# Kernel tuning notes

Measured on AMD Instinct MI355X. Metric: run time of the kernel, lower is better.

The kernel has to match this reference:

```python
import jax, jax.numpy as jnp
import numpy as np

EMBED_DIM = 256
N_COMPONENTS = 50
SIGMA = 1.0
B, N = 4, 4096


def setup_inputs() -> dict:
    key = jax.random.key(0)
    ks = jax.random.split(key, 7)
    d1, d2 = EMBED_DIM // 2, EMBED_DIM // 4  # 128, 64
    s = lambda fan_in: 1.0 / np.sqrt(fan_in)
    return {
        "embeddings": jax.random.normal(ks[0], (B, N, EMBED_DIM), dtype=jnp.float32),
        "W1": jax.random.uniform(ks[1], (EMBED_DIM, d1), jnp.float32, -s(EMBED_DIM), s(EMBED_DIM)),
        "b1": jax.random.uniform(ks[2], (d1,), jnp.float32, -s(EMBED_DIM), s(EMBED_DIM)),
        "W2": jax.random.uniform(ks[3], (d1, d2), jnp.float32, -s(d1), s(d1)),
        "b2": jax.random.uniform(ks[4], (d2,), jnp.float32, -s(d1), s(d1)),
        "W3": jax.random.uniform(ks[5], (d2, N_COMPONENTS), jnp.float32, -s(d2), s(d2)),
        "b3": jax.random.uniform(ks[6], (N_COMPONENTS,), jnp.float32, -s(d2), s(d2)),
    }


def reference(embeddings, W1, b1, W2, b2, W3, b3):
    # MLP projection: embed_dim -> embed_dim//2 -> embed_dim//4 -> n_components
    h = jax.nn.relu(jnp.einsum("bnd,df->bnf", embeddings, W1) + b1)
    h = jax.nn.relu(jnp.einsum("bnd,df->bnf", h, W2) + b2)
    z = jnp.einsum("bnd,df->bnf", h, W3) + b3  # (B, N, n_components)

    # Gaussian kernel from pairwise squared L2 distances: ||a-b||^2 = |a|^2 + |b|^2 - 2 a.b
    sq = jnp.sum(z * z, axis=-1)  # (B, N)
    dist = sq[:, :, None] + sq[:, None, :] - 2.0 * jnp.einsum("bik,bjk->bij", z, z)
    dist = jnp.maximum(dist, 0.0)
    kernel = jnp.exp(-dist / (2.0 * SIGMA ** 2))  # (B, N, N)

    # directed matrix: softmax over last dim, add epsilon, renormalize
    directed = jax.nn.softmax(kernel / SIGMA, axis=-1)
    directed = directed + 1e-6
    directed = directed / jnp.sum(directed, axis=-1, keepdims=True)
    return directed
```

## Files before the change

### kernel.cpp

```cpp
#include <hip/hip_runtime.h>
#include <cstdint>

#define ED 256
#define D1 128
#define D2 64
#define NC 50
#define NB 4
#define NN 4096
#define R1 16
#define TIB 8
#define JT 8
#define PTH 512

__global__ __launch_bounds__(256) void mlp_kernel(
    const float* __restrict__ emb,
    const float* __restrict__ W1, const float* __restrict__ b1,
    const float* __restrict__ W2, const float* __restrict__ b2,
    const float* __restrict__ W3, const float* __restrict__ b3,
    float* __restrict__ zT, float* __restrict__ sq)
{
    __shared__ __align__(16) float se[R1*ED];
    __shared__ __align__(16) float sh1[R1*D1];
    __shared__ __align__(16) float sh2[R1*D2];
    __shared__ __align__(16) float sz[R1*NC];
    const int t = threadIdx.x;
    const long row0 = (long)blockIdx.x * R1;

    {
        const float4* g4 = (const float4*)(emb + row0*ED);
        float4* s4 = (float4*)se;
        #pragma unroll
        for (int k = 0; k < (R1*ED/4)/256; k++)
            s4[t + k*256] = g4[t + k*256];
    }
    __syncthreads();

    {
        const int f = t & (D1-1);
        const int half = t >> 7;
        float acc[8];
        const float bias = b1[f];
        #pragma unroll
        for (int rr = 0; rr < 8; rr++) acc[rr] = bias;
        for (int d = 0; d < ED; d += 4) {
            const float w0 = W1[(d+0)*D1 + f];
            const float w1 = W1[(d+1)*D1 + f];
            const float w2 = W1[(d+2)*D1 + f];
            const float w3 = W1[(d+3)*D1 + f];
            #pragma unroll
            for (int rr = 0; rr < 8; rr++) {
                const float4 e = *(const float4*)&se[(half*8+rr)*ED + d];
                acc[rr] = fmaf(e.x, w0, acc[rr]);
                acc[rr] = fmaf(e.y, w1, acc[rr]);
                acc[rr] = fmaf(e.z, w2, acc[rr]);
                acc[rr] = fmaf(e.w, w3, acc[rr]);
            }
        }
        #pragma unroll
        for (int rr = 0; rr < 8; rr++)
            sh1[(half*8+rr)*D1 + f] = fmaxf(acc[rr], 0.0f);
    }
    __syncthreads();

    {
        const int f = t & (D2-1);
        const int g = t >> 6;
        float acc[4];
        const float bias = b2[f];
        #pragma unroll
        for (int rr = 0; rr < 4; rr++) acc[rr] = bias;
        for (int d = 0; d < D1; d += 4) {
            const float w0 = W2[(d+0)*D2 + f];
            const float w1 = W2[(d+1)*D2 + f];
            const float w2_ = W2[(d+2)*D2 + f];
            const float w3 = W2[(d+3)*D2 + f];
            #pragma unroll
            for (int rr = 0; rr < 4; rr++) {
                const float4 h = *(const float4*)&sh1[(g*4+rr)*D1 + d];
                acc[rr] = fmaf(h.x, w0, acc[rr]);
                acc[rr] = fmaf(h.y, w1, acc[rr]);
                acc[rr] = fmaf(h.z, w2_, acc[rr]);
                acc[rr] = fmaf(h.w, w3, acc[rr]);
            }
        }
        #pragma unroll
        for (int rr = 0; rr < 4; rr++)
            sh2[(g*4+rr)*D2 + f] = fmaxf(acc[rr], 0.0f);
    }
    __syncthreads();

    const int bb = (int)(row0 / NN);
    const int n0 = (int)(row0 - (long)bb*NN);
    for (int item = t; item < R1*NC; item += 256) {
        const int r = item / NC;
        const int f = item - r*NC;
        float acc = b3[f];
        for (int d = 0; d < D2; d++)
            acc = fmaf(sh2[r*D2 + d], W3[d*NC + f], acc);
        sz[r*NC + f] = acc;
        zT[((size_t)bb*NC + f)*NN + n0 + r] = acc;
    }
    __syncthreads();

    if (t < R1) {
        float s = 0.0f;
        #pragma unroll
        for (int k = 0; k < NC; k++) { const float v = sz[t*NC + k]; s = fmaf(v, v, s); }
        sq[row0 + t] = s;
    }
}

__global__ __launch_bounds__(PTH) void pair_kernel(
    const float* __restrict__ zT, const float* __restrict__ sq,
    float* __restrict__ out)
{
    const int t = threadIdx.x;
    const int b = blockIdx.x >> 9;
    const int i0 = (blockIdx.x & 511) * TIB;

    __shared__ __align__(16) float szi[NC][TIB];
    __shared__ float wsum[PTH/64][TIB];
    __shared__ float sS[TIB];

    const float* ztb = zT + (size_t)b * NC * NN;

    for (int idx = t; idx < NC*TIB; idx += PTH) {
        const int k = idx >> 3, ii = idx & 7;
        szi[k][ii] = ztb[(size_t)k*NN + i0 + ii];
    }
    __syncthreads();

    float acc[TIB][JT];
    #pragma unroll
    for (int ii = 0; ii < TIB; ii++)
        #pragma unroll
        for (int jj = 0; jj < JT; jj++) acc[ii][jj] = 0.0f;

    const int j0 = t * 4;
    #pragma unroll 5
    for (int k = 0; k < NC; k++) {
        const float4 zj0 = *(const float4*)(ztb + (size_t)k*NN + j0);
        const float4 zj1 = *(const float4*)(ztb + (size_t)k*NN + j0 + 2048);
        const float4 zia = *(const float4*)&szi[k][0];
        const float4 zib = *(const float4*)&szi[k][4];
        const float zi[8] = {zia.x, zia.y, zia.z, zia.w, zib.x, zib.y, zib.z, zib.w};
        const float zj[8] = {zj0.x, zj0.y, zj0.z, zj0.w, zj1.x, zj1.y, zj1.z, zj1.w};
        #pragma unroll
        for (int ii = 0; ii < TIB; ii++)
            #pragma unroll
            for (int jj = 0; jj < JT; jj++)
                acc[ii][jj] = fmaf(zi[ii], zj[jj], acc[ii][jj]);
    }

    const float* sqb = sq + (size_t)b * NN;
    float sqi[TIB];
    #pragma unroll
    for (int ii = 0; ii < TIB; ii++) sqi[ii] = sqb[i0 + ii];
    const float4 sja = *(const float4*)(sqb + j0);
    const float4 sjb = *(const float4*)(sqb + j0 + 2048);
    const float sqj[8] = {sja.x, sja.y, sja.z, sja.w, sjb.x, sjb.y, sjb.z, sjb.w};

    float rsum[TIB];
    #pragma unroll
    for (int ii = 0; ii < TIB; ii++) {
        float s = 0.0f;
        #pragma unroll
        for (int jj = 0; jj < JT; jj++) {
            const float d = fmaxf(sqi[ii] + sqj[jj] - 2.0f*acc[ii][jj], 0.0f);
            const float e = __expf(__expf(-0.5f*d));
            acc[ii][jj] = e;
            s += e;
        }
        rsum[ii] = s;
    }

    #pragma unroll
    for (int off = 32; off; off >>= 1)
        #pragma unroll
        for (int ii = 0; ii < TIB; ii++)
            rsum[ii] += __shfl_xor(rsum[ii], off, 64);
    const int wave = t >> 6, lane = t & 63;
    if (lane == 0) {
        #pragma unroll
        for (int ii = 0; ii < TIB; ii++) wsum[wave][ii] = rsum[ii];
    }
    __syncthreads();
    if (t < TIB) {
        float s = 0.0f;
        #pragma unroll
        for (int w = 0; w < PTH/64; w++) s += wsum[w][t];
        sS[t] = s;
    }
    __syncthreads();

    const float rn = 1.0f / (1.0f + (float)NN * 1e-6f);
    const float c = 1e-6f * rn;
    float* ob = out + ((size_t)(b*NN + i0)) * NN;
    #pragma unroll
    for (int ii = 0; ii < TIB; ii++) {
        const float is = rn / sS[ii];
        float4 v0, v1;
        v0.x = fmaf(acc[ii][0], is, c);
        v0.y = fmaf(acc[ii][1], is, c);
        v0.z = fmaf(acc[ii][2], is, c);
        v0.w = fmaf(acc[ii][3], is, c);
        v1.x = fmaf(acc[ii][4], is, c);
        v1.y = fmaf(acc[ii][5], is, c);
        v1.z = fmaf(acc[ii][6], is, c);
        v1.w = fmaf(acc[ii][7], is, c);
        *(float4*)(ob + (size_t)ii*NN + j0) = v0;
        *(float4*)(ob + (size_t)ii*NN + j0 + 2048) = v1;
    }
}

extern "C" void kernel_launch(void* const* d_in, const int* in_sizes, int n_in,
                              void* d_out, int out_size, void* d_ws, size_t ws_size,
                              hipStream_t stream) {
    const float* emb = (const float*)d_in[0];
    const float* W1  = (const float*)d_in[1];
    const float* b1  = (const float*)d_in[2];
    const float* W2  = (const float*)d_in[3];
    const float* b2  = (const float*)d_in[4];
    const float* W3  = (const float*)d_in[5];
    const float* b3  = (const float*)d_in[6];
    float* out = (float*)d_out;

    float* zT = (float*)d_ws;
    float* sq = zT + (size_t)NB*NC*NN;

    mlp_kernel<<<NB*NN/R1, 256, 0, stream>>>(emb, W1, b1, W2, b2, W3, b3, zT, sq);
    pair_kernel<<<NB*(NN/TIB), PTH, 0, stream>>>(zT, sq, out);
}
```

Measured before the change: 406.0 us.

## Retile pair kernel to 16 rows per block, prefetch z_j, coalesce zT stores

The pair kernel now covers 16 i-rows per block with 1024 threads, each handling 4 j-columns, instead of 8 rows with 8 columns per thread. Each z_j value loaded from global memory is therefore reused across twice as many rows, and every output row is written as one contiguous stretch. The next k-slice of z_j is software-prefetched in a register, and the i-row squared norms are staged in shared memory. The MLP kernel first stores z to shared memory, then writes the transposed zT with coalesced index order. The cost is a larger block and a launch-bounds occupancy hint, plus an unused prefetch read past the end of each batch's slice on the final iteration.

```diff
diff --git a/kernel.cpp b/kernel.cpp
--- a/kernel.cpp
+++ b/kernel.cpp
@@ -8,9 +8,9 @@
 #define NB 4
 #define NN 4096
 #define R1 16
-#define TIB 8
-#define JT 8
-#define PTH 512
+#define TIB 16
+#define JT 4
+#define PTH 1024
 
 __global__ __launch_bounds__(256) void mlp_kernel(
     const float* __restrict__ emb,
@@ -89,18 +89,23 @@
     }
     __syncthreads();
 
-    const int bb = (int)(row0 / NN);
-    const int n0 = (int)(row0 - (long)bb*NN);
     for (int item = t; item < R1*NC; item += 256) {
         const int r = item / NC;
         const int f = item - r*NC;
         float acc = b3[f];
         for (int d = 0; d < D2; d++)
             acc = fmaf(sh2[r*D2 + d], W3[d*NC + f], acc);
-        sz[r*NC + f] = acc;
-        zT[((size_t)bb*NC + f)*NN + n0 + r] = acc;
-    }
-    __syncthreads();
+        sz[item] = acc;
+    }
+    __syncthreads();
+
+    const int bb = (int)(row0 / NN);
+    const int n0 = (int)(row0 - (long)bb*NN);
+    for (int idx = t; idx < NC*R1; idx += 256) {
+        const int f = idx >> 4;
+        const int r = idx & 15;
+        zT[((size_t)bb*NC + f)*NN + n0 + r] = sz[r*NC + f];
+    }
 
     if (t < R1) {
         float s = 0.0f;
@@ -110,24 +115,27 @@
     }
 }
 
-__global__ __launch_bounds__(PTH) void pair_kernel(
+__global__ __launch_bounds__(PTH, 4) void pair_kernel(
     const float* __restrict__ zT, const float* __restrict__ sq,
     float* __restrict__ out)
 {
     const int t = threadIdx.x;
-    const int b = blockIdx.x >> 9;
-    const int i0 = (blockIdx.x & 511) * TIB;
+    const int b = blockIdx.x >> 8;
+    const int i0 = (blockIdx.x & 255) * TIB;
 
     __shared__ __align__(16) float szi[NC][TIB];
+    __shared__ float ssqi[TIB];
     __shared__ float wsum[PTH/64][TIB];
     __shared__ float sS[TIB];
 
     const float* ztb = zT + (size_t)b * NC * NN;
+    const float* sqb = sq + (size_t)b * NN;
 
     for (int idx = t; idx < NC*TIB; idx += PTH) {
-        const int k = idx >> 3, ii = idx & 7;
+        const int k = idx >> 4, ii = idx & 15;
         szi[k][ii] = ztb[(size_t)k*NN + i0 + ii];
     }
+    if (t < TIB) ssqi[t] = sqb[i0 + t];
     __syncthreads();
 
     float acc[TIB][JT];
@@ -137,36 +145,35 @@
         for (int jj = 0; jj < JT; jj++) acc[ii][jj] = 0.0f;
 
     const int j0 = t * 4;
-    #pragma unroll 5
+    float4 zj = *(const float4*)(ztb + j0);
     for (int k = 0; k < NC; k++) {
-        const float4 zj0 = *(const float4*)(ztb + (size_t)k*NN + j0);
-        const float4 zj1 = *(const float4*)(ztb + (size_t)k*NN + j0 + 2048);
+        const float4 zjn = *(const float4*)(ztb + (size_t)(k+1)*NN + j0);
         const float4 zia = *(const float4*)&szi[k][0];
         const float4 zib = *(const float4*)&szi[k][4];
-        const float zi[8] = {zia.x, zia.y, zia.z, zia.w, zib.x, zib.y, zib.z, zib.w};
-        const float zj[8] = {zj0.x, zj0.y, zj0.z, zj0.w, zj1.x, zj1.y, zj1.z, zj1.w};
+        const float4 zic = *(const float4*)&szi[k][8];
+        const float4 zid = *(const float4*)&szi[k][12];
+        const float zi[16] = {zia.x, zia.y, zia.z, zia.w, zib.x, zib.y, zib.z, zib.w,
+                              zic.x, zic.y, zic.z, zic.w, zid.x, zid.y, zid.z, zid.w};
+        const float zjv[4] = {zj.x, zj.y, zj.z, zj.w};
         #pragma unroll
         for (int ii = 0; ii < TIB; ii++)
             #pragma unroll
             for (int jj = 0; jj < JT; jj++)
-                acc[ii][jj] = fmaf(zi[ii], zj[jj], acc[ii][jj]);
-    }
-
-    const float* sqb = sq + (size_t)b * NN;
-    float sqi[TIB];
-    #pragma unroll
-    for (int ii = 0; ii < TIB; ii++) sqi[ii] = sqb[i0 + ii];
-    const float4 sja = *(const float4*)(sqb + j0);
-    const float4 sjb = *(const float4*)(sqb + j0 + 2048);
-    const float sqj[8] = {sja.x, sja.y, sja.z, sja.w, sjb.x, sjb.y, sjb.z, sjb.w};
+                acc[ii][jj] = fmaf(zi[ii], zjv[jj], acc[ii][jj]);
+        zj = zjn;
+    }
+
+    const float4 sj4 = *(const float4*)(sqb + j0);
+    const float sqj[4] = {sj4.x, sj4.y, sj4.z, sj4.w};
 
     float rsum[TIB];
     #pragma unroll
     for (int ii = 0; ii < TIB; ii++) {
+        const float sqi = ssqi[ii];
         float s = 0.0f;
         #pragma unroll
         for (int jj = 0; jj < JT; jj++) {
-            const float d = fmaxf(sqi[ii] + sqj[jj] - 2.0f*acc[ii][jj], 0.0f);
+            const float d = fmaxf(sqi + sqj[jj] - 2.0f*acc[ii][jj], 0.0f);
             const float e = __expf(__expf(-0.5f*d));
             acc[ii][jj] = e;
             s += e;
@@ -195,21 +202,16 @@
 
     const float rn = 1.0f / (1.0f + (float)NN * 1e-6f);
     const float c = 1e-6f * rn;
-    float* ob = out + ((size_t)(b*NN + i0)) * NN;
+    float* ob = out + ((size_t)(b*NN + i0)) * NN + j0;
     #pragma unroll
     for (int ii = 0; ii < TIB; ii++) {
         const float is = rn / sS[ii];
-        float4 v0, v1;
-        v0.x = fmaf(acc[ii][0], is, c);
-        v0.y = fmaf(acc[ii][1], is, c);
-        v0.z = fmaf(acc[ii][2], is, c);
-        v0.w = fmaf(acc[ii][3], is, c);
-        v1.x = fmaf(acc[ii][4], is, c);
-        v1.y = fmaf(acc[ii][5], is, c);
-        v1.z = fmaf(acc[ii][6], is, c);
-        v1.w = fmaf(acc[ii][7], is, c);
-        *(float4*)(ob + (size_t)ii*NN + j0) = v0;
-        *(float4*)(ob + (size_t)ii*NN + j0 + 2048) = v1;
+        float4 v;
+        v.x = fmaf(acc[ii][0], is, c);
+        v.y = fmaf(acc[ii][1], is, c);
+        v.z = fmaf(acc[ii][2], is, c);
+        v.w = fmaf(acc[ii][3], is, c);
+        *(float4*)(ob + (size_t)ii*NN) = v;
     }
 }
 
```

New measurement: 416.7 us. 1.03x slower.
